# Kernel optimization log

Measured on AMD Instinct MI355X. Metric: run time of the kernel, lower is better.

## Reference

```python
import jax, jax.numpy as jnp
import numpy as np

B, S, D, E = 4, 4096, 1024, 8
TOP_K = 2


def setup_inputs() -> dict:
    key = jax.random.key(0)
    k_x, k_gw, k_gb, k_ew, k_eb = jax.random.split(key, 5)
    x = jax.random.normal(k_x, (B, S, D), dtype=jnp.float32)
    gate_w = jax.random.normal(k_gw, (E, D), dtype=jnp.float32) * 0.02
    gate_b = jax.random.normal(k_gb, (E,), dtype=jnp.float32) * 0.02
    expert_w = jax.random.normal(k_ew, (E, D, D), dtype=jnp.float32) * 0.02
    expert_b = jax.random.normal(k_eb, (E, D), dtype=jnp.float32) * 0.02
    return {"x": x, "gate_w": gate_w, "gate_b": gate_b,
            "expert_w": expert_w, "expert_b": expert_b}


def reference(x, gate_w, gate_b, expert_w, expert_b):
    b, s, d = x.shape
    h = x.reshape(-1, d)                                  # [T, D]
    # router: linear -> softmax (fp32) -> top-k -> renormalize
    router_logits = h @ gate_w.T + gate_b                 # [T, E]
    probs = jax.nn.softmax(router_logits.astype(jnp.float32), axis=-1)
    topw, sel = jax.lax.top_k(probs, TOP_K)               # [T, K]
    topw = topw / jnp.sum(topw, axis=-1, keepdims=True)
    topw = topw.astype(h.dtype)
    out = jnp.zeros_like(h)
    for e in range(E):  # small fixed loop over experts
        # per-token combine weight for expert e (0 if not selected)
        we = jnp.sum(jnp.where(sel == e, topw, 0.0), axis=-1)  # [T]
        out = out + (h @ expert_w[e].T + expert_b[e]) * we[:, None]
    return out.reshape(b, s, d), router_logits
```

## Files before the change

kernel.cpp:

```cpp
#include <hip/hip_runtime.h>
#include <hip/hip_bf16.h>

typedef unsigned short u16;
typedef unsigned int u32;

#define T_TOK 16384
#define DIM   1024
#define NEXP  8

#define XB_OFF      0
#define WB_OFF      33554432
#define CNT_OFF     50331648
#define LIST_OFF    50332160
#define SELW_OFF    50856448
#define CONTRIB_OFF 51380736
#define WS_NEED     118489600ULL

__device__ __forceinline__ u16 f2bf(float f) {
    u32 u = __float_as_uint(f);
    u += 0x7fff + ((u >> 16) & 1);
    return (u16)(u >> 16);
}
__device__ __forceinline__ float bf2f(u16 u) {
    return __uint_as_float(((u32)u) << 16);
}

#define RT_PB 32

__global__ __launch_bounds__(256) void k_router(
    const float* __restrict__ x, const float* __restrict__ gw,
    const float* __restrict__ gb, float* __restrict__ logits,
    u16* __restrict__ xb, int* __restrict__ counts,
    int* __restrict__ lists, float4* __restrict__ selw,
    const float* __restrict__ ew, u16* __restrict__ wb)
{
    const int tid  = threadIdx.x;
    const int lane = tid & 63;
    const int w    = tid >> 6;

    __shared__ int   s_sel0[RT_PB], s_sel1[RT_PB];
    __shared__ int   s_lcnt[NEXP], s_gbase[NEXP];

    if (tid < NEXP) s_lcnt[tid] = 0;

    for (int i = 0; i < 8; ++i) {
        const int l = w * 8 + i;
        const int t = blockIdx.x * RT_PB + l;

        const float* xr = x + (size_t)t * DIM;
        float4 xs[4];
#pragma unroll
        for (int j = 0; j < 4; ++j)
            xs[j] = *reinterpret_cast<const float4*>(xr + (j * 64 + lane) * 4);

        float acc[NEXP];
#pragma unroll
        for (int e = 0; e < NEXP; ++e) {
            const float* gr = gw + e * DIM;
            float s = 0.f;
#pragma unroll
            for (int j = 0; j < 4; ++j) {
                float4 g = *reinterpret_cast<const float4*>(gr + (j * 64 + lane) * 4);
                s += xs[j].x * g.x + xs[j].y * g.y + xs[j].z * g.z + xs[j].w * g.w;
            }
            acc[e] = s;
        }
#pragma unroll
        for (int off = 1; off < 64; off <<= 1) {
#pragma unroll
            for (int e = 0; e < NEXP; ++e) acc[e] += __shfl_xor(acc[e], off);
        }
#pragma unroll
        for (int e = 0; e < NEXP; ++e) acc[e] += gb[e];

        int i0 = 0; float v0 = acc[0];
#pragma unroll
        for (int e = 1; e < NEXP; ++e) if (acc[e] > v0) { v0 = acc[e]; i0 = e; }
        int i1 = -1; float v1 = -3.4e38f;
#pragma unroll
        for (int e = 0; e < NEXP; ++e) if (e != i0 && acc[e] > v1) { v1 = acc[e]; i1 = e; }
        float e1  = __expf(v1 - v0);
        float inv = 1.f / (1.f + e1);
        float w0 = inv, w1 = e1 * inv;

        u16* xrow = xb + (size_t)t * DIM;
#pragma unroll
        for (int j = 0; j < 4; ++j) {
            int c = (j * 64 + lane) * 4;
            float4 v = xs[j];
            ushort4 u;
            u.x = f2bf(v.x); u.y = f2bf(v.y); u.z = f2bf(v.z); u.w = f2bf(v.w);
            *reinterpret_cast<ushort4*>(xrow + c) = u;
        }
        if (lane == 0) {
            float4 lo = make_float4(acc[0], acc[1], acc[2], acc[3]);
            float4 hi = make_float4(acc[4], acc[5], acc[6], acc[7]);
            *reinterpret_cast<float4*>(logits + (size_t)t * NEXP)     = lo;
            *reinterpret_cast<float4*>(logits + (size_t)t * NEXP + 4) = hi;
            selw[t] = make_float4(__int_as_float(i0), __int_as_float(i1), w0, w1);
            s_sel0[l] = i0; s_sel1[l] = i1;
        }
    }
    __syncthreads();

    int i0 = 0, i1 = 0, r0 = 0, r1 = 0;
    if (tid < RT_PB) {
        i0 = s_sel0[tid]; i1 = s_sel1[tid];
        r0 = atomicAdd(&s_lcnt[i0], 1);
        r1 = atomicAdd(&s_lcnt[i1], 1);
    }
    __syncthreads();
    if (tid < NEXP)
        s_gbase[tid] = atomicAdd(&counts[tid * 16], s_lcnt[tid]);
    __syncthreads();
    if (tid < RT_PB) {
        int t  = blockIdx.x * RT_PB + tid;
        lists[i0 * T_TOK + s_gbase[i0] + r0] = t * 2;
        lists[i1 * T_TOK + s_gbase[i1] + r1] = t * 2 + 1;
    }

    const int n4 = NEXP * DIM * DIM / 4;
    const int stride = gridDim.x * 256;
    for (int i = blockIdx.x * 256 + tid; i < n4; i += stride) {
        float4 v = reinterpret_cast<const float4*>(ew)[i];
        ushort4 u;
        u.x = f2bf(v.x); u.y = f2bf(v.y); u.z = f2bf(v.z); u.w = f2bf(v.w);
        reinterpret_cast<ushort4*>(wb)[i] = u;
    }
}


typedef __attribute__((ext_vector_type(8))) short bf16x8;
typedef __attribute__((ext_vector_type(4))) float f32x4;

#define GLDS16(g, l) __builtin_amdgcn_global_load_lds( \
    (const __attribute__((address_space(1))) void*)(g), \
    (__attribute__((address_space(3))) void*)(l), 16, 0, 0)

#define BAR() __builtin_amdgcn_s_barrier()
#define PRIO1() __builtin_amdgcn_s_setprio(1)
#define PRIO0() __builtin_amdgcn_s_setprio(0)
#define VMW4() asm volatile("s_waitcnt vmcnt(4)" ::: "memory")
#define VMW0() asm volatile("s_waitcnt vmcnt(0)" ::: "memory")

template<int ATOMIC>
__global__ __launch_bounds__(256, 3) void k_gemm(
    const u16* __restrict__ xb, const u16* __restrict__ wb,
    const int* __restrict__ counts, const int* __restrict__ lists,
    const float4* __restrict__ selw, u16* __restrict__ contrib,
    float* __restrict__ out)
{
    __shared__ u16 lds[24576];

    const int bid = (blockIdx.x & 7) * 1024 + (blockIdx.x >> 3);
    const int e   = bid >> 10;
    const int mt  = (bid >> 3) & 127;
    const int nt  = bid & 7;
    const int cnt = counts[e * 16];
    if (mt * 128 >= cnt) return;

    const int tid  = threadIdx.x;
    const int lane = tid & 63;
    const int wid  = tid >> 6;
    const int wm   = wid >> 1;
    const int wn   = wid & 1;
    const int listbase = e * T_TOK;

    const int s0 = ((int)(blockIdx.x >> 3) * 11) & 31;

    const int srow = tid >> 2;
    const int cA   = (((tid & 3) - (tid >> 3)) & 3) * 8;
    int tokA[2];
#pragma unroll
    for (int l = 0; l < 2; ++l) {
        int slot = mt * 128 + l * 64 + srow;
        tokA[l] = lists[listbase + (slot < cnt ? slot : cnt - 1)] >> 1;
    }
    const u16* srcA0 = xb + (size_t)tokA[0] * DIM + cA;
    const u16* srcA1 = xb + (size_t)tokA[1] * DIM + cA;
    const u16* srcB0 = wb + ((size_t)e << 20) + (size_t)(nt * 128 + srow) * DIM + cA;
    const u16* srcB1 = srcB0 + (size_t)64 * DIM;

#define STAGE(b, kk) do { \
    GLDS16(srcA0 + (kk), &lds[(b) * 8192 + wid * 512]); \
    GLDS16(srcA1 + (kk), &lds[(b) * 8192 + 2048 + wid * 512]); \
    GLDS16(srcB0 + (kk), &lds[(b) * 8192 + 4096 + wid * 512]); \
    GLDS16(srcB1 + (kk), &lds[(b) * 8192 + 4096 + 2048 + wid * 512]); } while (0)

    const int cs8  = (((lane >> 4) + ((lane >> 1) & 3)) & 3) * 8;
    const int offA = (wm * 64 + (lane & 15)) * 32 + cs8;
    const int offB = 4096 + (wn * 64 + (lane & 15)) * 32 + cs8;

    bf16x8 Af[4], Bf[4];
    f32x4 acc[4][4];
#pragma unroll
    for (int mi = 0; mi < 4; ++mi)
#pragma unroll
        for (int ni = 0; ni < 4; ++ni) acc[mi][ni] = (f32x4)0.f;

#define LDA4(b) do { \
    Af[0] = *(const bf16x8*)&lds[(b) * 8192 + 0 * 512 + offA]; \
    Af[1] = *(const bf16x8*)&lds[(b) * 8192 + 1 * 512 + offA]; \
    Af[2] = *(const bf16x8*)&lds[(b) * 8192 + 2 * 512 + offA]; \
    Af[3] = *(const bf16x8*)&lds[(b) * 8192 + 3 * 512 + offA]; } while (0)
#define LDB4(b) do { \
    Bf[0] = *(const bf16x8*)&lds[(b) * 8192 + 0 * 512 + offB]; \
    Bf[1] = *(const bf16x8*)&lds[(b) * 8192 + 1 * 512 + offB]; \
    Bf[2] = *(const bf16x8*)&lds[(b) * 8192 + 2 * 512 + offB]; \
    Bf[3] = *(const bf16x8*)&lds[(b) * 8192 + 3 * 512 + offB]; } while (0)
#define MFMA_ROW(i) do { \
    acc[i][0] = __builtin_amdgcn_mfma_f32_16x16x32_bf16(Af[i], Bf[0], acc[i][0], 0, 0, 0); \
    acc[i][1] = __builtin_amdgcn_mfma_f32_16x16x32_bf16(Af[i], Bf[1], acc[i][1], 0, 0, 0); \
    acc[i][2] = __builtin_amdgcn_mfma_f32_16x16x32_bf16(Af[i], Bf[2], acc[i][2], 0, 0, 0); \
    acc[i][3] = __builtin_amdgcn_mfma_f32_16x16x32_bf16(Af[i], Bf[3], acc[i][3], 0, 0, 0); } while (0)
#define MFMA16() do { MFMA_ROW(0); MFMA_ROW(1); MFMA_ROW(2); MFMA_ROW(3); } while (0)

#define PHASE(p, b, sb) do { \
    if ((p) < 30) STAGE(sb, ((s0 + (p) + 2) & 31) * 32); \
    LDA4(b); LDB4(b); \
    PRIO1(); MFMA16(); PRIO0(); \
    if ((p) < 30) { VMW4(); } else { VMW0(); } \
    if ((p) < 31) BAR(); \
} while (0)

    STAGE(0, (s0 & 31) * 32);
    STAGE(1, ((s0 + 1) & 31) * 32);
    VMW4(); BAR();

    for (int j = 0; j < 10; ++j) {
        PHASE(j * 3 + 0, 0, 2);
        PHASE(j * 3 + 1, 1, 0);
        PHASE(j * 3 + 2, 2, 1);
    }
    PHASE(30, 0, 2);
    PHASE(31, 1, 0);

    const int rbase = (lane >> 4) * 4;
    const int cbase = nt * 128 + wn * 64 + (lane & 15);
#pragma unroll
    for (int mi = 0; mi < 4; ++mi) {
#pragma unroll
        for (int r = 0; r < 4; ++r) {
            int slot = mt * 128 + wm * 64 + mi * 16 + rbase + r;
            if (slot < cnt) {
                int lv = lists[listbase + slot];
                if (ATOMIC) {
                    int tok = lv >> 1;
                    float4 sw = selw[tok];
                    float wgt = (lv & 1) ? sw.w : sw.z;
                    float* orow = out + (size_t)tok * DIM + cbase;
#pragma unroll
                    for (int ni = 0; ni < 4; ++ni)
                        atomicAdd(orow + ni * 16, acc[mi][ni][r] * wgt);
                } else {
                    u16* crow = contrib + (size_t)lv * DIM + cbase;
#pragma unroll
                    for (int ni = 0; ni < 4; ++ni)
                        crow[ni * 16] = f2bf(acc[mi][ni][r]);
                }
            }
        }
    }
}

__global__ __launch_bounds__(256) void k_combine(
    const u16* __restrict__ contrib, const float4* __restrict__ selw,
    const float* __restrict__ eb, float* __restrict__ out)
{
    const int lane = threadIdx.x & 63;
    const int t    = blockIdx.x * 4 + (threadIdx.x >> 6);
    float4 sw = selw[t];
    const int e0 = __float_as_int(sw.x);
    const int e1 = __float_as_int(sw.y);
    const float w0 = sw.z, w1 = sw.w;
    const u16* c0 = contrib + (size_t)(t * 2) * DIM;
    const u16* c1 = c0 + DIM;
    const float* b0 = eb + e0 * DIM;
    const float* b1 = eb + e1 * DIM;
    float* orow = out + (size_t)t * DIM;
#pragma unroll
    for (int j = 0; j < 2; ++j) {
        const int c = (j * 64 + lane) * 8;
        uint4 u0 = *reinterpret_cast<const uint4*>(c0 + c);
        uint4 u1 = *reinterpret_cast<const uint4*>(c1 + c);
        const u16* p0 = (const u16*)&u0;
        const u16* p1 = (const u16*)&u1;
#pragma unroll
        for (int h = 0; h < 2; ++h) {
            float4 bb0 = *reinterpret_cast<const float4*>(b0 + c + h * 4);
            float4 bb1 = *reinterpret_cast<const float4*>(b1 + c + h * 4);
            float4 o;
            o.x = w0 * (bf2f(p0[h*4+0]) + bb0.x) + w1 * (bf2f(p1[h*4+0]) + bb1.x);
            o.y = w0 * (bf2f(p0[h*4+1]) + bb0.y) + w1 * (bf2f(p1[h*4+1]) + bb1.y);
            o.z = w0 * (bf2f(p0[h*4+2]) + bb0.z) + w1 * (bf2f(p1[h*4+2]) + bb1.z);
            o.w = w0 * (bf2f(p0[h*4+3]) + bb0.w) + w1 * (bf2f(p1[h*4+3]) + bb1.w);
            *reinterpret_cast<float4*>(orow + c + h * 4) = o;
        }
    }
}

__global__ __launch_bounds__(256) void k_bias(
    const float4* __restrict__ selw, const float* __restrict__ eb,
    float* __restrict__ out)
{
    const int lane = threadIdx.x & 63;
    const int t    = blockIdx.x * 4 + (threadIdx.x >> 6);
    float4 sw = selw[t];
    const float* b0 = eb + __float_as_int(sw.x) * DIM;
    const float* b1 = eb + __float_as_int(sw.y) * DIM;
    float* orow = out + (size_t)t * DIM;
#pragma unroll
    for (int j = 0; j < 4; ++j) {
        int c = (j * 64 + lane) * 4;
        float4 f0 = *reinterpret_cast<const float4*>(b0 + c);
        float4 f1 = *reinterpret_cast<const float4*>(b1 + c);
        float4 o;
        o.x = sw.z * f0.x + sw.w * f1.x;
        o.y = sw.z * f0.y + sw.w * f1.y;
        o.z = sw.z * f0.z + sw.w * f1.z;
        o.w = sw.z * f0.w + sw.w * f1.w;
        *reinterpret_cast<float4*>(orow + c) = o;
    }
}

extern "C" void kernel_launch(void* const* d_in, const int* in_sizes, int n_in,
                              void* d_out, int out_size, void* d_ws, size_t ws_size,
                              hipStream_t stream) {
    const float* x  = (const float*)d_in[0];
    const float* gw = (const float*)d_in[1];
    const float* gb = (const float*)d_in[2];
    const float* ew = (const float*)d_in[3];
    const float* eb = (const float*)d_in[4];

    float* out    = (float*)d_out;
    float* logits = out + (size_t)T_TOK * DIM;

    char*   ws      = (char*)d_ws;
    u16*    xb      = (u16*)(ws + XB_OFF);
    u16*    wb      = (u16*)(ws + WB_OFF);
    int*    counts  = (int*)(ws + CNT_OFF);
    int*    lists   = (int*)(ws + LIST_OFF);
    float4* selw    = (float4*)(ws + SELW_OFF);
    u16*    contrib = (u16*)(ws + CONTRIB_OFF);

    hipMemsetAsync((void*)(ws + CNT_OFF), 0, 512, stream);
    k_router<<<T_TOK / RT_PB, 256, 0, stream>>>(x, gw, gb, logits, xb, counts,
                                                lists, selw, ew, wb);

    const int grid = NEXP * 128 * 8;
    if (ws_size >= WS_NEED) {
        k_gemm<0><<<grid, 256, 0, stream>>>(xb, wb, counts, lists, selw, contrib, out);
        k_combine<<<T_TOK / 4, 256, 0, stream>>>(contrib, selw, eb, out);
    } else {
        k_bias<<<T_TOK / 4, 256, 0, stream>>>(selw, eb, out);
        k_gemm<1><<<grid, 256, 0, stream>>>(xb, wb, counts, lists, selw, contrib, out);
    }
}
```

Measured before the change: 162.5 us.

## Enlarge expert GEMM tile to 256x256 with 512-thread blocks

The grouped expert GEMM moves from 128x128 tiles with 4 waves to 256x256 tiles with 8 waves. Each wave now holds a 128x64 accumulator and loads A fragments in two halves, which raises arithmetic intensity per LDS and global load. The per-block K-start rotation (s0) is dropped, so all blocks begin at k=0. In exchange the kernel uses more registers and LDS, tile padding waste grows for experts with ragged token counts, and the grid is 4x smaller, so occupancy and load balance across CUs may suffer.

```diff
diff --git a/kernel.cpp b/kernel.cpp
--- a/kernel.cpp
+++ b/kernel.cpp
@@ -144,87 +144,89 @@
 #define VMW0() asm volatile("s_waitcnt vmcnt(0)" ::: "memory")
 
 template<int ATOMIC>
-__global__ __launch_bounds__(256, 3) void k_gemm(
+__global__ __launch_bounds__(512, 2) void k_gemm(
     const u16* __restrict__ xb, const u16* __restrict__ wb,
     const int* __restrict__ counts, const int* __restrict__ lists,
     const float4* __restrict__ selw, u16* __restrict__ contrib,
     float* __restrict__ out)
 {
-    __shared__ u16 lds[24576];
-
-    const int bid = (blockIdx.x & 7) * 1024 + (blockIdx.x >> 3);
-    const int e   = bid >> 10;
-    const int mt  = (bid >> 3) & 127;
-    const int nt  = bid & 7;
+    __shared__ u16 lds[49152];
+
+    const int bid = (blockIdx.x & 7) * 256 + (blockIdx.x >> 3);
+    const int e   = bid >> 8;
+    const int mt  = (bid >> 2) & 63;
+    const int nt  = bid & 3;
     const int cnt = counts[e * 16];
-    if (mt * 128 >= cnt) return;
+    if (mt * 256 >= cnt) return;
 
     const int tid  = threadIdx.x;
     const int lane = tid & 63;
     const int wid  = tid >> 6;
-    const int wm   = wid >> 1;
-    const int wn   = wid & 1;
+    const int wm   = wid >> 2;
+    const int wn   = wid & 3;
     const int listbase = e * T_TOK;
-
-    const int s0 = ((int)(blockIdx.x >> 3) * 11) & 31;
 
     const int srow = tid >> 2;
     const int cA   = (((tid & 3) - (tid >> 3)) & 3) * 8;
     int tokA[2];
 #pragma unroll
     for (int l = 0; l < 2; ++l) {
-        int slot = mt * 128 + l * 64 + srow;
+        int slot = mt * 256 + l * 128 + srow;
         tokA[l] = lists[listbase + (slot < cnt ? slot : cnt - 1)] >> 1;
     }
     const u16* srcA0 = xb + (size_t)tokA[0] * DIM + cA;
     const u16* srcA1 = xb + (size_t)tokA[1] * DIM + cA;
-    const u16* srcB0 = wb + ((size_t)e << 20) + (size_t)(nt * 128 + srow) * DIM + cA;
-    const u16* srcB1 = srcB0 + (size_t)64 * DIM;
+    const u16* srcB0 = wb + ((size_t)e << 20) + (size_t)(nt * 256 + srow) * DIM + cA;
+    const u16* srcB1 = srcB0 + (size_t)128 * DIM;
 
 #define STAGE(b, kk) do { \
-    GLDS16(srcA0 + (kk), &lds[(b) * 8192 + wid * 512]); \
-    GLDS16(srcA1 + (kk), &lds[(b) * 8192 + 2048 + wid * 512]); \
-    GLDS16(srcB0 + (kk), &lds[(b) * 8192 + 4096 + wid * 512]); \
-    GLDS16(srcB1 + (kk), &lds[(b) * 8192 + 4096 + 2048 + wid * 512]); } while (0)
+    GLDS16(srcA0 + (kk), &lds[(b) * 16384 + wid * 512]); \
+    GLDS16(srcA1 + (kk), &lds[(b) * 16384 + 4096 + wid * 512]); \
+    GLDS16(srcB0 + (kk), &lds[(b) * 16384 + 8192 + wid * 512]); \
+    GLDS16(srcB1 + (kk), &lds[(b) * 16384 + 12288 + wid * 512]); } while (0)
 
     const int cs8  = (((lane >> 4) + ((lane >> 1) & 3)) & 3) * 8;
-    const int offA = (wm * 64 + (lane & 15)) * 32 + cs8;
-    const int offB = 4096 + (wn * 64 + (lane & 15)) * 32 + cs8;
+    const int offA = wm * 4096 + (lane & 15) * 32 + cs8;
+    const int offB = 8192 + wn * 2048 + (lane & 15) * 32 + cs8;
 
     bf16x8 Af[4], Bf[4];
-    f32x4 acc[4][4];
-#pragma unroll
-    for (int mi = 0; mi < 4; ++mi)
+    f32x4 acc[8][4];
+#pragma unroll
+    for (int mi = 0; mi < 8; ++mi)
 #pragma unroll
         for (int ni = 0; ni < 4; ++ni) acc[mi][ni] = (f32x4)0.f;
 
-#define LDA4(b) do { \
-    Af[0] = *(const bf16x8*)&lds[(b) * 8192 + 0 * 512 + offA]; \
-    Af[1] = *(const bf16x8*)&lds[(b) * 8192 + 1 * 512 + offA]; \
-    Af[2] = *(const bf16x8*)&lds[(b) * 8192 + 2 * 512 + offA]; \
-    Af[3] = *(const bf16x8*)&lds[(b) * 8192 + 3 * 512 + offA]; } while (0)
+#define LDA4(b, q) do { \
+    Af[0] = *(const bf16x8*)&lds[(b) * 16384 + ((q) * 4 + 0) * 512 + offA]; \
+    Af[1] = *(const bf16x8*)&lds[(b) * 16384 + ((q) * 4 + 1) * 512 + offA]; \
+    Af[2] = *(const bf16x8*)&lds[(b) * 16384 + ((q) * 4 + 2) * 512 + offA]; \
+    Af[3] = *(const bf16x8*)&lds[(b) * 16384 + ((q) * 4 + 3) * 512 + offA]; } while (0)
 #define LDB4(b) do { \
-    Bf[0] = *(const bf16x8*)&lds[(b) * 8192 + 0 * 512 + offB]; \
-    Bf[1] = *(const bf16x8*)&lds[(b) * 8192 + 1 * 512 + offB]; \
-    Bf[2] = *(const bf16x8*)&lds[(b) * 8192 + 2 * 512 + offB]; \
-    Bf[3] = *(const bf16x8*)&lds[(b) * 8192 + 3 * 512 + offB]; } while (0)
-#define MFMA_ROW(i) do { \
-    acc[i][0] = __builtin_amdgcn_mfma_f32_16x16x32_bf16(Af[i], Bf[0], acc[i][0], 0, 0, 0); \
-    acc[i][1] = __builtin_amdgcn_mfma_f32_16x16x32_bf16(Af[i], Bf[1], acc[i][1], 0, 0, 0); \
-    acc[i][2] = __builtin_amdgcn_mfma_f32_16x16x32_bf16(Af[i], Bf[2], acc[i][2], 0, 0, 0); \
-    acc[i][3] = __builtin_amdgcn_mfma_f32_16x16x32_bf16(Af[i], Bf[3], acc[i][3], 0, 0, 0); } while (0)
-#define MFMA16() do { MFMA_ROW(0); MFMA_ROW(1); MFMA_ROW(2); MFMA_ROW(3); } while (0)
+    Bf[0] = *(const bf16x8*)&lds[(b) * 16384 + 0 * 512 + offB]; \
+    Bf[1] = *(const bf16x8*)&lds[(b) * 16384 + 1 * 512 + offB]; \
+    Bf[2] = *(const bf16x8*)&lds[(b) * 16384 + 2 * 512 + offB]; \
+    Bf[3] = *(const bf16x8*)&lds[(b) * 16384 + 3 * 512 + offB]; } while (0)
+#define MFMA16(q) do { \
+    _Pragma("unroll") \
+    for (int i = 0; i < 4; ++i) { \
+        acc[(q)*4+i][0] = __builtin_amdgcn_mfma_f32_16x16x32_bf16(Af[i], Bf[0], acc[(q)*4+i][0], 0, 0, 0); \
+        acc[(q)*4+i][1] = __builtin_amdgcn_mfma_f32_16x16x32_bf16(Af[i], Bf[1], acc[(q)*4+i][1], 0, 0, 0); \
+        acc[(q)*4+i][2] = __builtin_amdgcn_mfma_f32_16x16x32_bf16(Af[i], Bf[2], acc[(q)*4+i][2], 0, 0, 0); \
+        acc[(q)*4+i][3] = __builtin_amdgcn_mfma_f32_16x16x32_bf16(Af[i], Bf[3], acc[(q)*4+i][3], 0, 0, 0); \
+    } } while (0)
 
 #define PHASE(p, b, sb) do { \
-    if ((p) < 30) STAGE(sb, ((s0 + (p) + 2) & 31) * 32); \
-    LDA4(b); LDB4(b); \
-    PRIO1(); MFMA16(); PRIO0(); \
+    if ((p) < 30) STAGE(sb, ((p) + 2) * 32); \
+    LDB4(b); LDA4(b, 0); \
+    PRIO1(); MFMA16(0); PRIO0(); \
+    LDA4(b, 1); \
+    PRIO1(); MFMA16(1); PRIO0(); \
     if ((p) < 30) { VMW4(); } else { VMW0(); } \
     if ((p) < 31) BAR(); \
 } while (0)
 
-    STAGE(0, (s0 & 31) * 32);
-    STAGE(1, ((s0 + 1) & 31) * 32);
+    STAGE(0, 0);
+    STAGE(1, 32);
     VMW4(); BAR();
 
     for (int j = 0; j < 10; ++j) {
@@ -236,12 +238,12 @@
     PHASE(31, 1, 0);
 
     const int rbase = (lane >> 4) * 4;
-    const int cbase = nt * 128 + wn * 64 + (lane & 15);
-#pragma unroll
-    for (int mi = 0; mi < 4; ++mi) {
+    const int cbase = nt * 256 + wn * 64 + (lane & 15);
+#pragma unroll
+    for (int mi = 0; mi < 8; ++mi) {
 #pragma unroll
         for (int r = 0; r < 4; ++r) {
-            int slot = mt * 128 + wm * 64 + mi * 16 + rbase + r;
+            int slot = mt * 256 + wm * 128 + mi * 16 + rbase + r;
             if (slot < cnt) {
                 int lv = lists[listbase + slot];
                 if (ATOMIC) {
@@ -347,12 +349,12 @@
     k_router<<<T_TOK / RT_PB, 256, 0, stream>>>(x, gw, gb, logits, xb, counts,
                                                 lists, selw, ew, wb);
 
-    const int grid = NEXP * 128 * 8;
+    const int grid = NEXP * 64 * 4;
     if (ws_size >= WS_NEED) {
-        k_gemm<0><<<grid, 256, 0, stream>>>(xb, wb, counts, lists, selw, contrib, out);
+        k_gemm<0><<<grid, 512, 0, stream>>>(xb, wb, counts, lists, selw, contrib, out);
         k_combine<<<T_TOK / 4, 256, 0, stream>>>(contrib, selw, eb, out);
     } else {
         k_bias<<<T_TOK / 4, 256, 0, stream>>>(selw, eb, out);
-        k_gemm<1><<<grid, 256, 0, stream>>>(xb, wb, counts, lists, selw, contrib, out);
-    }
-}
+        k_gemm<1><<<grid, 512, 0, stream>>>(xb, wb, counts, lists, selw, contrib, out);
+    }
+}
```

New measurement: 172.7 us. 1.06x slower.
